# Optimization experiments

Measured on AMD Instinct MI355X. Metric: run time of the kernel, lower is better.

## Reference

```python
import jax, jax.numpy as jnp
import numpy as np

BATCH = 4096      # batch_size per the module __init__
TEMP = 0.5        # temperature
WORLD = 1         # world_size (single device; GatherLayer path skipped)
D = 128           # projection-head embedding dim
EPS = 1e-8        # torch CosineSimilarity eps


def _neg_indices(N, half):
    # Static mask from mask_correlated_samples: remove diagonal and the
    # (i, half+i)/(half+i, i) entries; each row keeps exactly N-2 columns.
    mask = np.ones((N, N), dtype=bool)
    np.fill_diagonal(mask, False)
    r = np.arange(half)
    mask[r, half + r] = False
    mask[half + r, r] = False
    return np.nonzero(mask)[1].reshape(N, N - 2)  # row-major -> per-row sorted cols


def setup_inputs() -> dict:
    key = jax.random.key(0)
    k1, k2 = jax.random.split(key)
    z_i = jax.random.normal(k1, (BATCH, D), dtype=jnp.float32)
    z_j = jax.random.normal(k2, (BATCH, D), dtype=jnp.float32)
    return {"z_i": z_i, "z_j": z_j}


def reference(z_i, z_j):
    half = BATCH * WORLD
    N = 2 * half
    z = jnp.concatenate([z_i, z_j], axis=0)                       # (N, D)
    zn = z / jnp.maximum(jnp.linalg.norm(z, axis=1, keepdims=True), EPS)
    # reordered_z = cat(z[half:], z[:half]) == roll by -half
    rn = jnp.roll(zn, -half, axis=0)
    # cosine-sim matrix via single GEMM instead of (N,1,D)x(1,N,D) broadcast
    sim = (zn @ rn.T) / TEMP                                       # (N, N)

    i = jnp.arange(half)
    sim_i_j = sim[i, i + half]          # torch.diag(sim, +half)
    sim_j_i = sim[i + half, i]          # torch.diag(sim, -half)
    pos = jnp.concatenate([sim_i_j, sim_j_i])[:, None]             # (N, 1)

    neg_idx = jnp.asarray(_neg_indices(N, half))                   # (N, N-2) static
    neg = jnp.take_along_axis(sim, neg_idx, axis=1)                # (N, N-2)

    logits = jnp.concatenate([pos, neg], axis=1)                   # (N, N-1)
    # CrossEntropy with labels=0, reduction='sum', then / N
    loss = jnp.sum(jax.nn.logsumexp(logits, axis=1) - logits[:, 0]) / N
    return loss
```

## Files before the change

### kernel.cpp

```cpp
#include <hip/hip_runtime.h>

#define HALF   4096
#define NROWS  8192
#define DDIM   128
#define NGROUPS (NROWS / 128)
#define NPAIRS  (NGROUPS * (NGROUPS + 1) / 2)
#define LDS_STRIDE 272

typedef _Float16 v8h __attribute__((ext_vector_type(8)));
typedef _Float16 v2h __attribute__((ext_vector_type(2)));
typedef float    v4f __attribute__((ext_vector_type(4)));

#if __has_builtin(__builtin_amdgcn_exp2f)
#define EXP2F(x) __builtin_amdgcn_exp2f(x)
#else
#define EXP2F(x) exp2f(x)
#endif
#if __has_builtin(__builtin_amdgcn_logf)
#define LOG2F(x) __builtin_amdgcn_logf(x)
#else
#define LOG2F(x) __log2f(x)
#endif

#define CEXP 2.8853900817779268f

__global__ __launch_bounds__(256) void nt_normalize(
        const float* __restrict__ z_i, const float* __restrict__ z_j,
        _Float16* __restrict__ zn, float* __restrict__ S) {
    int tid  = threadIdx.x;
    int lane = tid & 63;
    int row  = blockIdx.x * 4 + (tid >> 6);
    if (tid < 4) S[blockIdx.x * 4 + tid] = 0.f;

    const float* src = (row < HALF) ? (z_i + (size_t)row * DDIM)
                                    : (z_j + (size_t)(row - HALF) * DDIM);
    float2 v = *(const float2*)(src + lane * 2);
    float ss = v.x * v.x + v.y * v.y;
    #pragma unroll
    for (int off = 32; off >= 1; off >>= 1)
        ss += __shfl_xor(ss, off, 64);
    float inv = 1.0f / fmaxf(sqrtf(ss), 1e-8f);
    v2h p;
    p.x = (_Float16)(v.x * inv);
    p.y = (_Float16)(v.y * inv);
    *(v2h*)(zn + (size_t)row * DDIM + lane * 2) = p;
}

__global__ __launch_bounds__(256, 4) void nt_gram_sym(
        const _Float16* __restrict__ zn, float* __restrict__ S,
        float* __restrict__ P) {
    __shared__ unsigned char lds[128 * LDS_STRIDE];
    __shared__ float cs[4][128];

    int tid  = threadIdx.x;
    int lane = tid & 63;
    int w    = tid >> 6;
    int quad = lane >> 4;
    int cl   = lane & 15;

    int p = blockIdx.x;
    int J = (int)((sqrtf(8.0f * (float)p + 1.0f) - 1.0f) * 0.5f);
    while ((J + 1) * (J + 2) / 2 <= p) ++J;
    while (J * (J + 1) / 2 > p) --J;
    int I = p - J * (J + 1) / 2;
    int r0 = I * 128, c0 = J * 128;
    bool offdiag = (I != J);
    bool ppart   = (J == I + 32);

    v8h a[2][4];
    #pragma unroll
    for (int u = 0; u < 2; ++u) {
        int arow = r0 + w * 32 + u * 16 + cl;
        #pragma unroll
        for (int t = 0; t < 4; ++t)
            a[u][t] = *(const v8h*)(zn + (size_t)arow * DDIM + t * 32 + quad * 8);
    }

    const uint4* gb = (const uint4*)zn;
    #pragma unroll
    for (int i = 0; i < 8; ++i) {
        int rr = (tid >> 4) + i * 16;
        uint4 v = gb[(size_t)(c0 + rr) * 16 + (tid & 15)];
        *(uint4*)&lds[(size_t)rr * LDS_STRIDE + (tid & 15) * 16] = v;
    }
    __syncthreads();

    float sums[2][4] = {{0.f,0.f,0.f,0.f},{0.f,0.f,0.f,0.f}};

    #pragma unroll
    for (int sub = 0; sub < 8; ++sub) {
        v4f acc0 = {0.f, 0.f, 0.f, 0.f};
        v4f acc1 = {0.f, 0.f, 0.f, 0.f};
        #pragma unroll
        for (int t = 0; t < 4; ++t) {
            v8h b = *(const v8h*)&lds[(size_t)(sub * 16 + cl) * LDS_STRIDE + t * 64 + quad * 16];
            acc0 = __builtin_amdgcn_mfma_f32_16x16x32_f16(a[0][t], b, acc0, 0, 0, 0);
            acc1 = __builtin_amdgcn_mfma_f32_16x16x32_f16(a[1][t], b, acc1, 0, 0, 0);
        }
        float cp = 0.f;
        #pragma unroll
        for (int r = 0; r < 4; ++r) {
            float e0 = EXP2F(fmaf(acc0[r], CEXP, -CEXP));
            float e1 = EXP2F(fmaf(acc1[r], CEXP, -CEXP));
            sums[0][r] += e0;
            sums[1][r] += e1;
            cp += e0 + e1;
            if (ppart && cl == quad * 4 + r) {
                if (sub == w * 2)     P[r0 + w * 32 +      quad * 4 + r] = e0;
                if (sub == w * 2 + 1) P[r0 + w * 32 + 16 + quad * 4 + r] = e1;
            }
        }
        if (offdiag) {
            cp += __shfl_xor(cp, 16, 64);
            cp += __shfl_xor(cp, 32, 64);
            if (quad == 0)
                cs[w][sub * 16 + cl] = cp;
        }
    }

    #pragma unroll
    for (int u = 0; u < 2; ++u)
        #pragma unroll
        for (int r = 0; r < 4; ++r) {
            float s = sums[u][r];
            #pragma unroll
            for (int off = 1; off < 16; off <<= 1)
                s += __shfl_xor(s, off, 64);
            if (cl == 0)
                atomicAdd(&S[r0 + w * 32 + u * 16 + quad * 4 + r], s);
        }

    if (offdiag) {
        __syncthreads();
        if (tid < 128) {
            float c = cs[0][tid] + cs[1][tid] + cs[2][tid] + cs[3][tid];
            atomicAdd(&S[c0 + tid], c);
        }
    }
}

__global__ __launch_bounds__(1024) void nt_correct(
        const float* __restrict__ S, const float* __restrict__ P,
        float* __restrict__ out) {
    int tid = threadIdx.x;
    float part = 0.f;
    #pragma unroll
    for (int k = 0; k < 4; ++k) {
        int pr = tid + k * 1024;
        float e = P[pr];
        part += LOG2F(S[pr] - e) + LOG2F(S[pr + HALF] - e);
    }
    #pragma unroll
    for (int off = 32; off >= 1; off >>= 1)
        part += __shfl_xor(part, off, 64);
    __shared__ float red[16];
    if ((tid & 63) == 0) red[tid >> 6] = part;
    __syncthreads();
    if (tid == 0) {
        float t = 0.f;
        #pragma unroll
        for (int i = 0; i < 16; ++i) t += red[i];
        out[0] = t * (0.69314718055994531f / (float)NROWS);
    }
}

extern "C" void kernel_launch(void* const* d_in, const int* in_sizes, int n_in,
                              void* d_out, int out_size, void* d_ws, size_t ws_size,
                              hipStream_t stream) {
    const float* z_i = (const float*)d_in[0];
    const float* z_j = (const float*)d_in[1];
    _Float16* zn  = (_Float16*)d_ws;
    float*    S   = (float*)((char*)d_ws + (size_t)NROWS * DDIM * 2);
    float*    P   = S + NROWS;
    float*    out = (float*)d_out;

    nt_normalize<<<dim3(NROWS / 4), dim3(256), 0, stream>>>(z_i, z_j, zn, S);
    nt_gram_sym<<<dim3(NPAIRS), dim3(256), 0, stream>>>(zn, S, P);
    nt_correct<<<dim3(1), dim3(1024), 0, stream>>>(S, P, out);
}
```

Before: 82.29 us.

## Replace row-sum atomics with per-tile scratch partials and parallel tail reduction

The Gram kernel no longer does global float atomics into S for row and column sums. Each tile instead writes its 128 row partials and 128 column partials to a 64x64x128 scratch buffer. A new 32-block tail kernel sums those partials per row pair, computes the log terms, and finishes with an atomic accumulator plus a last-block counter, replacing the single-block correction kernel. This removes atomic contention and the serial tail, at the cost of about 2 MB of extra scratch writes and reads.

```diff
diff --git a/kernel.cpp b/kernel.cpp
--- a/kernel.cpp
+++ b/kernel.cpp
@@ -26,11 +26,11 @@
 
 __global__ __launch_bounds__(256) void nt_normalize(
         const float* __restrict__ z_i, const float* __restrict__ z_j,
-        _Float16* __restrict__ zn, float* __restrict__ S) {
+        _Float16* __restrict__ zn, unsigned* __restrict__ acccnt) {
     int tid  = threadIdx.x;
     int lane = tid & 63;
     int row  = blockIdx.x * 4 + (tid >> 6);
-    if (tid < 4) S[blockIdx.x * 4 + tid] = 0.f;
+    if (blockIdx.x == 0 && tid < 2) acccnt[tid] = 0u;
 
     const float* src = (row < HALF) ? (z_i + (size_t)row * DDIM)
                                     : (z_j + (size_t)(row - HALF) * DDIM);
@@ -47,10 +47,11 @@
 }
 
 __global__ __launch_bounds__(256, 4) void nt_gram_sym(
-        const _Float16* __restrict__ zn, float* __restrict__ S,
+        const _Float16* __restrict__ zn, float* __restrict__ scratch,
         float* __restrict__ P) {
     __shared__ unsigned char lds[128 * LDS_STRIDE];
     __shared__ float cs[4][128];
+    __shared__ float rsum[128];
 
     int tid  = threadIdx.x;
     int lane = tid & 63;
@@ -127,40 +128,62 @@
             for (int off = 1; off < 16; off <<= 1)
                 s += __shfl_xor(s, off, 64);
             if (cl == 0)
-                atomicAdd(&S[r0 + w * 32 + u * 16 + quad * 4 + r], s);
-        }
-
-    if (offdiag) {
-        __syncthreads();
-        if (tid < 128) {
+                rsum[w * 32 + u * 16 + quad * 4 + r] = s;
+        }
+
+    __syncthreads();
+    if (tid < 128) {
+        scratch[((size_t)I * 64 + J) * 128 + tid] = rsum[tid];
+        if (offdiag) {
             float c = cs[0][tid] + cs[1][tid] + cs[2][tid] + cs[3][tid];
-            atomicAdd(&S[c0 + tid], c);
-        }
-    }
-}
-
-__global__ __launch_bounds__(1024) void nt_correct(
-        const float* __restrict__ S, const float* __restrict__ P,
+            scratch[((size_t)J * 64 + I) * 128 + tid] = c;
+        }
+    }
+}
+
+__global__ __launch_bounds__(256) void nt_tail(
+        const float* __restrict__ scratch, const float* __restrict__ P,
+        float* __restrict__ accf, unsigned* __restrict__ cnt,
         float* __restrict__ out) {
     int tid = threadIdx.x;
+    int b   = blockIdx.x;
+    int col = tid & 127;
+    int h   = tid >> 7;
+
+    float s0 = 0.f, s1 = 0.f;
+    #pragma unroll
+    for (int i = 0; i < 32; ++i) {
+        int t = h * 32 + i;
+        s0 += scratch[((size_t)(b      * 64 + t)) * 128 + col];
+        s1 += scratch[((size_t)((b+32) * 64 + t)) * 128 + col];
+    }
+    __shared__ float t0[2][128], t1[2][128];
+    t0[h][col] = s0;
+    t1[h][col] = s1;
+    __syncthreads();
+
     float part = 0.f;
-    #pragma unroll
-    for (int k = 0; k < 4; ++k) {
-        int pr = tid + k * 1024;
-        float e = P[pr];
-        part += LOG2F(S[pr] - e) + LOG2F(S[pr + HALF] - e);
+    if (tid < 128) {
+        int pr   = b * 128 + tid;
+        float Sa = t0[0][tid] + t0[1][tid];
+        float Sb = t1[0][tid] + t1[1][tid];
+        float e  = P[pr];
+        part = LOG2F(Sa - e) + LOG2F(Sb - e);
     }
     #pragma unroll
     for (int off = 32; off >= 1; off >>= 1)
         part += __shfl_xor(part, off, 64);
-    __shared__ float red[16];
+    __shared__ float red[4];
     if ((tid & 63) == 0) red[tid >> 6] = part;
     __syncthreads();
     if (tid == 0) {
-        float t = 0.f;
-        #pragma unroll
-        for (int i = 0; i < 16; ++i) t += red[i];
-        out[0] = t * (0.69314718055994531f / (float)NROWS);
+        atomicAdd(accf, red[0] + red[1] + red[2] + red[3]);
+        __threadfence();
+        unsigned old = atomicAdd(cnt, 1u);
+        if (old == 31) {
+            float tot = atomicAdd(accf, 0.0f);
+            out[0] = tot * (0.69314718055994531f / (float)NROWS);
+        }
     }
 }
 
@@ -169,12 +192,15 @@
                               hipStream_t stream) {
     const float* z_i = (const float*)d_in[0];
     const float* z_j = (const float*)d_in[1];
-    _Float16* zn  = (_Float16*)d_ws;
-    float*    S   = (float*)((char*)d_ws + (size_t)NROWS * DDIM * 2);
-    float*    P   = S + NROWS;
-    float*    out = (float*)d_out;
-
-    nt_normalize<<<dim3(NROWS / 4), dim3(256), 0, stream>>>(z_i, z_j, zn, S);
-    nt_gram_sym<<<dim3(NPAIRS), dim3(256), 0, stream>>>(zn, S, P);
-    nt_correct<<<dim3(1), dim3(1024), 0, stream>>>(S, P, out);
-}
+    _Float16* zn      = (_Float16*)d_ws;
+    float*    P       = (float*)((char*)d_ws + (size_t)NROWS * DDIM * 2);
+    float*    scratch = P + HALF;
+    float*    accf    = scratch + (size_t)64 * 64 * 128;
+    unsigned* acccnt  = (unsigned*)accf;
+    unsigned* cnt     = acccnt + 1;
+    float*    out     = (float*)d_out;
+
+    nt_normalize<<<dim3(NROWS / 4), dim3(256), 0, stream>>>(z_i, z_j, zn, acccnt);
+    nt_gram_sym<<<dim3(NPAIRS), dim3(256), 0, stream>>>(zn, scratch, P);
+    nt_tail<<<dim3(32), dim3(256), 0, stream>>>(scratch, P, accf, cnt, out);
+}
```

Result: slower. 99.68 us (+21.1%).
